# Kernel tuning notes

Hardware: AMD Instinct MI355X
Metric: run time of the kernel (lower is better)

The kernel has to match this reference:

```python
import jax, jax.numpy as jnp
import numpy as np

B, S, HID = 1, 2048, 2048
H, KVH, D = 32, 8, 64
NUM_MASKS = 3
ROPE_THETA = 10000.0


def rope_tables(seq_len, dim, theta=ROPE_THETA):
    inv_freq = 1.0 / (theta ** (np.arange(0, dim, 2, dtype=np.float32) / dim))
    t = np.arange(seq_len, dtype=np.float32)
    freqs = np.outer(t, inv_freq)                      # [S, D/2]
    emb = np.concatenate([freqs, freqs], axis=-1)      # [S, D]
    return jnp.asarray(np.cos(emb))[None], jnp.asarray(np.sin(emb))[None]  # [1,S,D]


def setup_inputs() -> dict:
    key = jax.random.key(0)
    ks = jax.random.split(key, 5)
    cos, sin = rope_tables(S, D)
    sc = 1.0 / np.sqrt(HID)
    return {
        "hidden_states": jax.random.normal(ks[0], (B, S, HID), jnp.float32),
        "cos": cos, "sin": sin,
        "Wq": jax.random.normal(ks[1], (HID, H * D), jnp.float32) * sc,
        "Wk": jax.random.normal(ks[2], (HID, KVH * D), jnp.float32) * sc,
        "Wv": jax.random.normal(ks[3], (HID, KVH * D), jnp.float32) * sc,
        "Wo": jax.random.normal(ks[4], (H * D, HID), jnp.float32) * sc,
        "num_masks": NUM_MASKS,
    }


def rotate_half(x):
    x1, x2 = jnp.split(x, 2, axis=-1)
    return jnp.concatenate([-x2, x1], axis=-1)


def block_causal_bias(seq_len, num_mask, dtype):
    block_size = num_mask + 1
    i = jnp.arange(seq_len)[:, None]
    j = jnp.arange(seq_len)[None, :]
    causal = j <= i
    column = causal & (j % (num_mask + 1) == 0)
    block = causal & ((i // block_size) == (j // block_size))
    allowed = column | block
    neg = jnp.asarray(jnp.finfo(dtype).min if dtype != jnp.float32 else -jnp.inf, dtype)
    return jnp.where(allowed, jnp.asarray(0.0, dtype), neg)  # [S,S]


def reference(hidden_states, cos, sin, Wq, Wk, Wv, Wo, num_masks):
    b, s, _ = hidden_states.shape
    scaling = D ** -0.5
    # projections -> [B, heads, S, D]
    q = (hidden_states @ Wq).reshape(b, s, H, D).transpose(0, 2, 1, 3)
    k = (hidden_states @ Wk).reshape(b, s, KVH, D).transpose(0, 2, 1, 3)
    v = (hidden_states @ Wv).reshape(b, s, KVH, D).transpose(0, 2, 1, 3)
    # RoPE (cos/sin: [1,S,D] -> [1,1,S,D])
    c, sn = cos[:, None], sin[:, None]
    q = q * c + rotate_half(q) * sn
    k = k * c + rotate_half(k) * sn
    # GQA: repeat kv heads
    g = H // KVH
    k = jnp.repeat(k, g, axis=1)
    v = jnp.repeat(v, g, axis=1)
    bias = block_causal_bias(s, num_masks, hidden_states.dtype)  # [S,S]
    scores = jnp.einsum("bhqd,bhkd->bhqk", q, k) * scaling + bias[None, None]
    probs = jax.nn.softmax(scores, axis=-1)
    out = jnp.einsum("bhqk,bhkd->bhqd", probs, v)  # [B,H,S,D]
    out = out.transpose(0, 2, 1, 3).reshape(b, s, H * D)
    return out @ Wo
```

## Files before the change

### kernel.cpp

```cpp
#include <hip/hip_runtime.h>
#include <hip/hip_bf16.h>
#include <stdint.h>

#define S_LEN  2048
#define HIDDEN 2048
#define NH     32
#define NKVH   8
#define HD     64
#define NHD    (NH*HD)
#define KVD    (NKVH*HD)

typedef __attribute__((ext_vector_type(8))) short  short8;
typedef __attribute__((ext_vector_type(4))) short  short4v;
typedef __attribute__((ext_vector_type(4))) float  f32x4;
typedef __attribute__((ext_vector_type(4))) float  float4v;
typedef __attribute__((ext_vector_type(8))) __bf16 bf16x8;

__device__ __forceinline__ short f2bf(float x){
  uint32_t u = __builtin_bit_cast(uint32_t, x);
  u += 0x7fffu + ((u >> 16) & 1u);
  return (short)(u >> 16);
}

__device__ __forceinline__ f32x4 mfma_bf16(short8 a, short8 b, f32x4 c){
  return __builtin_amdgcn_mfma_f32_16x16x32_bf16(
      __builtin_bit_cast(bf16x8, a), __builtin_bit_cast(bf16x8, b), c, 0, 0, 0);
}

__device__ __forceinline__ void gload16(const short* g, short* l){
  __builtin_amdgcn_global_load_lds(
      (const __attribute__((address_space(1))) void*)g,
      (__attribute__((address_space(3))) void*)l, 16, 0, 0);
}

__global__ __launch_bounds__(256) void k_prep(const float* __restrict__ hs,
                                              short* __restrict__ hsb,
                                              const float* __restrict__ Wq, short* __restrict__ WqT,
                                              const float* __restrict__ Wk, short* __restrict__ WkT,
                                              const float* __restrict__ Wv, short* __restrict__ WvT,
                                              const float* __restrict__ Wo, short* __restrict__ WoT){
  int bid = blockIdx.x;
  if (bid < 4096){
    int i = bid*256 + threadIdx.x;
    float4v v = ((const float4v* __restrict__)hs)[i];
    short4v o;
#pragma unroll
    for (int j=0;j<4;j++) o[j] = f2bf(v[j]);
    ((short4v* __restrict__)hsb)[i] = o;
    return;
  }
  bid -= 4096;
  const float* W; short* WT; int R, C, GX;
  if (bid < 4096)      { W = Wq; WT = WqT; R = HIDDEN; C = NHD; GX = 64; }
  else if (bid < 5120) { bid -= 4096; W = Wk; WT = WkT; R = HIDDEN; C = KVD; GX = 16; }
  else if (bid < 6144) { bid -= 5120; W = Wv; WT = WvT; R = HIDDEN; C = KVD; GX = 16; }
  else                 { bid -= 6144; W = Wo; WT = WoT; R = NHD; C = HIDDEN; GX = 64; }
  const int bx = bid % GX, by = bid / GX;
  __shared__ float tile[32][33];
  const int x = threadIdx.x & 31, y0 = threadIdx.x >> 5;
  const int c0 = bx*32, r0 = by*32;
#pragma unroll
  for (int yy=y0; yy<32; yy+=8) tile[yy][x] = W[(size_t)(r0+yy)*C + c0 + x];
  __syncthreads();
#pragma unroll
  for (int yy=y0; yy<32; yy+=8) WT[(size_t)(c0+yy)*R + r0 + x] = f2bf(tile[x][yy]);
}

struct GemmIdx {
  int wid, r, g, wr, wc, kg, gtid;
};
__device__ __forceinline__ GemmIdx gemm_idx(){
  GemmIdx ix;
  int tid = threadIdx.x, lane = tid&63;
  ix.kg = tid>>8; ix.gtid = tid&255;
  ix.wid = (tid>>6)&3; ix.r = lane&15; ix.g = lane>>4;
  ix.wr = ix.wid>>1; ix.wc = ix.wid&1;
  return ix;
}

__device__ __forceinline__ void stage128(const short* gA, const short* gB,
                                         short* As, short* Bs, int kt, int w){
  const int K = HIDDEN;
  gload16(gA + kt*32,                As + w*512);
  gload16(gA + (size_t)64*K + kt*32, As + 2048 + w*512);
  gload16(gB + kt*32,                Bs + w*512);
  gload16(gB + (size_t)64*K + kt*32, Bs + 2048 + w*512);
}

__device__ __forceinline__ void compute128(const short* As, const short* Bs,
                                           f32x4 acc[4][4], const GemmIdx& ix){
  short8 af[4], bf[4];
#pragma unroll
  for (int m=0;m<4;m++) af[m] = *(const short8*)&As[(ix.wr*64 + m*16 + ix.r)*32 + ix.g*8];
#pragma unroll
  for (int n=0;n<4;n++) bf[n] = *(const short8*)&Bs[(ix.wc*64 + n*16 + ix.r)*32 + ix.g*8];
#pragma unroll
  for (int m=0;m<4;m++)
#pragma unroll
    for (int n=0;n<4;n++) acc[m][n] = mfma_bf16(af[m], bf[n], acc[m][n]);
}

template<int NKT>
__device__ __forceinline__ void gemm_core512(const short* __restrict__ A,
                                             const short* __restrict__ BT,
                                             int bm, int bn, int kbase, short* LDS,
                                             f32x4 acc[4][4], const GemmIdx& ix){
  const int K = HIDDEN;
  const short* gA = A  + (size_t)(bm*128 + (ix.gtid>>2))*K + kbase + ix.kg*(NKT*32) + (ix.gtid&3)*8;
  const short* gB = BT + (size_t)(bn*128 + (ix.gtid>>2))*K + kbase + ix.kg*(NKT*32) + (ix.gtid&3)*8;
  short* L   = LDS + ix.kg*16384;
  short* As0 = L;        short* Bs0 = L + 4096;
  short* As1 = L + 8192; short* Bs1 = L + 12288;
  const int w = ix.gtid>>6;

#pragma unroll
  for (int m=0;m<4;m++)
#pragma unroll
    for (int n=0;n<4;n++) acc[m][n] = (f32x4){0.f,0.f,0.f,0.f};

  stage128(gA, gB, As0, Bs0, 0, w);
  __syncthreads();
  for (int u=0; u<NKT/2; ++u){
    const int t = 2*u;
    if (t+1 < NKT) stage128(gA, gB, As1, Bs1, t+1, w);
    compute128(As0, Bs0, acc, ix);
    __syncthreads();
    if (t+2 < NKT) stage128(gA, gB, As0, Bs0, t+2, w);
    compute128(As1, Bs1, acc, ix);
    __syncthreads();
  }

  float* red = (float*)LDS;
  if (ix.kg){
#pragma unroll
    for (int m=0;m<4;m++)
#pragma unroll
      for (int n=0;n<4;n++)
#pragma unroll
        for (int j=0;j<4;j++)
          red[ix.wid*4096 + (m*16 + ix.g*4 + j)*64 + n*16 + ix.r] = acc[m][n][j];
  }
  __syncthreads();
  if (!ix.kg){
#pragma unroll
    for (int m=0;m<4;m++)
#pragma unroll
      for (int n=0;n<4;n++)
#pragma unroll
        for (int j=0;j<4;j++)
          acc[m][n][j] += red[ix.wid*4096 + (m*16 + ix.g*4 + j)*64 + n*16 + ix.r];
  }
}

__global__ __launch_bounds__(512, 4) void k_gemm_qkv(const short* __restrict__ hsb,
                                                     const short* __restrict__ WqT,
                                                     const short* __restrict__ WkT,
                                                     const short* __restrict__ WvT,
                                                     const float* __restrict__ cosT,
                                                     const float* __restrict__ sinT,
                                                     const int* __restrict__ nm,
                                                     short* __restrict__ Qb,
                                                     short* __restrict__ Kb,
                                                     short* __restrict__ VT,
                                                     short* __restrict__ VTs){
  __shared__ short LDS[32768];
  const int bn = blockIdx.x, bm = blockIdx.y;
  GemmIdx ix = gemm_idx();
  f32x4 acc[4][4];

  if (bn < 16){
    gemm_core512<32>(hsb, WqT + (size_t)bn*128*HIDDEN, bm, 0, 0, LDS, acc, ix);
    if (ix.kg) return;
    const int h2 = bn*2 + ix.wc;
#pragma unroll
    for (int m=0;m<4;m++)
#pragma unroll
      for (int j=0;j<4;j++){
        const int s = bm*128 + ix.wr*64 + m*16 + ix.g*4 + j;
        const float* cr = cosT + s*64;
        const float* sr = sinT + s*64;
#pragma unroll
        for (int n=0;n<2;n++){
          const int d = n*16 + ix.r;
          float x1 = acc[m][n][j], x2 = acc[m][n+2][j];
          Qb[(size_t)s*NHD + h2*64 + d]      = f2bf((x1*cr[d]    - x2*sr[d])   *0.125f);
          Qb[(size_t)s*NHD + h2*64 + d + 32] = f2bf((x2*cr[d+32] + x1*sr[d+32])*0.125f);
        }
      }
  } else if (bn < 20){
    gemm_core512<32>(hsb, WkT + (size_t)(bn-16)*128*HIDDEN, bm, 0, 0, LDS, acc, ix);
    if (ix.kg) return;
    const int h2 = (bn-16)*2 + ix.wc;
#pragma unroll
    for (int m=0;m<4;m++)
#pragma unroll
      for (int j=0;j<4;j++){
        const int s = bm*128 + ix.wr*64 + m*16 + ix.g*4 + j;
        const float* cr = cosT + s*64;
        const float* sr = sinT + s*64;
#pragma unroll
        for (int n=0;n<2;n++){
          const int d = n*16 + ix.r;
          float x1 = acc[m][n][j], x2 = acc[m][n+2][j];
          Kb[(size_t)s*KVD + h2*64 + d]      = f2bf(x1*cr[d]    - x2*sr[d]);
          Kb[(size_t)s*KVD + h2*64 + d + 32] = f2bf(x2*cr[d+32] + x1*sr[d+32]);
        }
      }
  } else {
    gemm_core512<32>(hsb, WvT + (size_t)(bn-20)*128*HIDDEN, bm, 0, 0, LDS, acc, ix);
    if (ix.kg) return;
    const int bs  = nm[0] + 1;
    const int c0  = (bn-20)*128 + ix.wc*64;
    const int s0b = bm*128 + ix.wr*64 + ix.g*4;
    const int md  = s0b % bs;
    const int b0  = (s0b - md)/bs;
    const int d16 = 16/bs;
    bool mj[4]; int tj[4];
#pragma unroll
    for (int j=0;j<4;j++){
      int v = md + j;
      mj[j] = (v==0)||(v==bs)||(v==2*bs)||(v==3*bs);
      tj[j] = (v>=3*bs)?3:((v>=2*bs)?2:((v>=bs)?1:0));
    }
#pragma unroll
    for (int m=0;m<4;m++){
      const int sm = s0b + m*16;
#pragma unroll
      for (int n=0;n<4;n++){
        const int d = c0 + n*16 + ix.r;
        short4v o;
#pragma unroll
        for (int j=0;j<4;j++) o[j] = f2bf(acc[m][n][j]);
        *(short4v*)&VT[(size_t)d*S_LEN + sm] = o;
#pragma unroll
        for (int j=0;j<4;j++)
          if (mj[j]) VTs[(size_t)d*S_LEN + b0 + m*d16 + tj[j]] = o[j];
      }
    }
  }
}

__global__ __launch_bounds__(512, 4) void k_gemm(const short* __restrict__ A,
                                                 const short* __restrict__ BT,
                                                 float* __restrict__ C, int Nc){
  __shared__ short LDS[32768];
  const int bn = blockIdx.x, bm = blockIdx.y;
  GemmIdx ix = gemm_idx();
  f32x4 acc[4][4];
  gemm_core512<32>(A, BT, bm, bn, 0, LDS, acc, ix);
  if (ix.kg) return;
#pragma unroll
  for (int m=0;m<4;m++)
#pragma unroll
    for (int n=0;n<4;n++)
#pragma unroll
      for (int j=0;j<4;j++)
        C[(size_t)(bm*128 + ix.wr*64 + m*16 + ix.g*4 + j)*Nc
          + bn*128 + ix.wc*64 + n*16 + ix.r] = acc[m][n][j];
}


__device__ __forceinline__ void sm_pv1(f32x4 sc[4],
                                       float mrow[4], float lrow[4],
                                       f32x4 acc[4], short* Pw,
                                       const short* Vtile,
                                       int r, int g){
#pragma unroll
  for (int j=0;j<4;j++){
    float v = fmaxf(fmaxf(sc[0][j], sc[1][j]), fmaxf(sc[2][j], sc[3][j]));
    v = fmaxf(v, __shfl_xor(v, 1));
    v = fmaxf(v, __shfl_xor(v, 2));
    v = fmaxf(v, __shfl_xor(v, 4));
    v = fmaxf(v, __shfl_xor(v, 8));
    float mn = fmaxf(mrow[j], v);
    float fac = __expf(mrow[j] - mn);
    mrow[j] = mn;
#pragma unroll
    for (int f=0;f<4;f++) acc[f][j] *= fac;
    float rs = 0.f;
#pragma unroll
    for (int n=0;n<4;n++){
      float p = __expf(sc[n][j] - mn);
      rs += p;
      sc[n][j] = p;
    }
    rs += __shfl_xor(rs, 1);
    rs += __shfl_xor(rs, 2);
    rs += __shfl_xor(rs, 4);
    rs += __shfl_xor(rs, 8);
    lrow[j] = lrow[j]*fac + rs;
  }
#pragma unroll
  for (int n=0;n<4;n++)
#pragma unroll
    for (int j=0;j<4;j++)
      Pw[(g*4+j)*72 + n*16 + r] = f2bf(sc[n][j]);

  short8 pf0 = *(short8*)&Pw[r*72 + g*8];
  short8 pf1 = *(short8*)&Pw[r*72 + 32 + g*8];
#pragma unroll
  for (int f=0;f<4;f++){
    short8 vf0 = *(const short8*)(Vtile + (size_t)(f*16 + r)*S_LEN + g*8);
    short8 vf1 = *(const short8*)(Vtile + (size_t)(f*16 + r)*S_LEN + 32 + g*8);
    acc[f] = mfma_bf16(pf0, vf0, acc[f]);
    acc[f] = mfma_bf16(pf1, vf1, acc[f]);
  }
}

__global__ __launch_bounds__(64, 4) void k_attn3(const short* __restrict__ Qb,
                                                 const short* __restrict__ Kb,
                                                 const short* __restrict__ VT,
                                                 const short* __restrict__ VTs,
                                                 const int* __restrict__ nm,
                                                 short* __restrict__ Ob){
  const int i  = gridDim.x - 1 - blockIdx.x;
  const int qs = i >> 5;
  const int h  = i & 31;
  const int hk = h >> 2;
  const int bs = nm[0] + 1;

  const int lane = threadIdx.x;
  const int r = lane&15, g = lane>>4;

  __shared__ short Pw[16*72];

  const int qlo = qs*16;

  short8 qf0 = *(const short8*)(Qb + (size_t)(qlo + r)*NHD + h*HD + g*8);
  short8 qf1 = *(const short8*)(Qb + (size_t)(qlo + r)*NHD + h*HD + 32 + g*8);

  f32x4 acc[4];
  float mrow[4], lrow[4];
#pragma unroll
  for (int f=0;f<4;f++) acc[f] = (f32x4){0.f,0.f,0.f,0.f};
#pragma unroll
  for (int j=0;j<4;j++){ mrow[j] = -1e30f; lrow[j] = 0.f; }

  const short* Kg  = Kb  + hk*HD;
  const short* Vsg = VTs + (size_t)hk*HD*S_LEN;
  const short* Vdg = VT  + (size_t)hk*HD*S_LEN;

  const int cmax = qlo / bs;
  const int nct = (cmax + 63) >> 6;
  for (int ct=0; ct<nct; ++ct){
    const int cbase = ct*64;
    f32x4 sc[4];
#pragma unroll
    for (int n=0;n<4;n++){
      const int key = bs*(cbase + n*16 + r);
      short8 kf0 = *(const short8*)(Kg + (size_t)key*KVD + g*8);
      short8 kf1 = *(const short8*)(Kg + (size_t)key*KVD + 32 + g*8);
      f32x4 z = (f32x4){0.f,0.f,0.f,0.f};
      z = mfma_bf16(qf0, kf0, z);
      sc[n] = mfma_bf16(qf1, kf1, z);
    }
    if (cmax - cbase < 64){
#pragma unroll
      for (int n=0;n<4;n++){
        if (cbase + n*16 + r >= cmax){
#pragma unroll
          for (int j=0;j<4;j++) sc[n][j] = -1e30f;
        }
      }
    }
    sm_pv1(sc, mrow, lrow, acc, Pw, Vsg + cbase, r, g);
  }

  {
    const int key = qlo + r;
    short8 kf0 = *(const short8*)(Kg + (size_t)key*KVD + g*8);
    short8 kf1 = *(const short8*)(Kg + (size_t)key*KVD + 32 + g*8);
    f32x4 z = (f32x4){0.f,0.f,0.f,0.f};
    z = mfma_bf16(qf0, kf0, z);
    f32x4 sc0 = mfma_bf16(qf1, kf1, z);

    const int rb = r / bs, rm = r % bs;
#pragma unroll
    for (int j=0;j<4;j++){
      const int qrel = g*4 + j;
      bool ok = (r <= qrel) && ((rm == 0) || (rb == qrel/bs));
      sc0[j] = ok ? sc0[j] : -1e30f;
    }

#pragma unroll
    for (int j=0;j<4;j++){
      float v = sc0[j];
      v = fmaxf(v, __shfl_xor(v, 1));
      v = fmaxf(v, __shfl_xor(v, 2));
      v = fmaxf(v, __shfl_xor(v, 4));
      v = fmaxf(v, __shfl_xor(v, 8));
      float mn = fmaxf(mrow[j], v);
      float fac = __expf(mrow[j] - mn);
      mrow[j] = mn;
#pragma unroll
      for (int f=0;f<4;f++) acc[f][j] *= fac;
      float p = __expf(sc0[j] - mn);
      sc0[j] = p;
      float rs = p;
      rs += __shfl_xor(rs, 1);
      rs += __shfl_xor(rs, 2);
      rs += __shfl_xor(rs, 4);
      rs += __shfl_xor(rs, 8);
      lrow[j] = lrow[j]*fac + rs;
    }
#pragma unroll
    for (int j=0;j<4;j++){
      Pw[(g*4+j)*72 + r]      = f2bf(sc0[j]);
      Pw[(g*4+j)*72 + 16 + r] = 0;
    }
    short8 pf0 = *(short8*)&Pw[r*72 + g*8];
#pragma unroll
    for (int f=0;f<4;f++){
      short8 vf0 = *(const short8*)(Vdg + (size_t)(f*16 + r)*S_LEN + qlo + g*8);
      acc[f] = mfma_bf16(pf0, vf0, acc[f]);
    }
  }

#pragma unroll
  for (int j=0;j<4;j++){
    float inv = 1.f / lrow[j];
    const int q = qlo + g*4 + j;
#pragma unroll
    for (int f=0;f<4;f++)
      Ob[(size_t)q*NHD + h*HD + f*16 + r] = f2bf(acc[f][j]*inv);
  }
}

extern "C" void kernel_launch(void* const* d_in, const int* in_sizes, int n_in,
                              void* d_out, int out_size, void* d_ws, size_t ws_size,
                              hipStream_t stream){
  const float* hs   = (const float*)d_in[0];
  const float* cosT = (const float*)d_in[1];
  const float* sinT = (const float*)d_in[2];
  const float* Wq   = (const float*)d_in[3];
  const float* Wk   = (const float*)d_in[4];
  const float* Wv   = (const float*)d_in[5];
  const float* Wo   = (const float*)d_in[6];
  const int*   nm   = (const int*)d_in[7];

  char* ws = (char*)d_ws;
  short* hsb  = (short*)(ws);
  short* WqT  = (short*)(ws + (8ull<<20));
  short* WkT  = (short*)(ws + (16ull<<20));
  short* WvT  = (short*)(ws + (18ull<<20));
  short* WoT  = (short*)(ws + (20ull<<20));
  short* Qb   = (short*)(ws + (28ull<<20));
  short* Kb   = (short*)(ws + (36ull<<20));
  short* VT   = (short*)(ws + (38ull<<20));
  short* VTs  = (short*)(ws + (40ull<<20));
  short* attnb= (short*)(ws + (42ull<<20));
  float* out  = (float*)d_out;

  k_prep<<<dim3(14336), 256, 0, stream>>>(hs, hsb, Wq, WqT, Wk, WkT, Wv, WvT, Wo, WoT);

  k_gemm_qkv<<<dim3(24, 16), 512, 0, stream>>>(hsb, WqT, WkT, WvT, cosT, sinT, nm,
                                               Qb, Kb, VT, VTs);

  k_attn3<<<dim3((S_LEN/16)*NH), 64, 0, stream>>>(Qb, Kb, VT, VTs, nm, attnb);

  k_gemm<<<dim3(NHD/128, S_LEN/128), 512, 0, stream>>>(attnb, WoT, out, HIDDEN);
}
```

Before: 136.2 us.

## Split-K four ways in output GEMM and stage V transpose through LDS

The output projection GEMM now uses 1024-thread blocks with four K-groups of 16 tiles each, reducing partial sums through LDS in sequence. This raises per-CU wave count for the 256-block grid, at the cost of extra reduction barriers and double the LDS. The V epilogue in the QKV kernel now writes the tile transposed into LDS, then emits coalesced 16-byte VT stores and a strided-gather VTs. The VTs path computes the block size with a log2, so it assumes the block size is a power of two.

```diff
diff --git a/kernel.cpp b/kernel.cpp
--- a/kernel.cpp
+++ b/kernel.cpp
@@ -100,14 +100,14 @@
     for (int n=0;n<4;n++) acc[m][n] = mfma_bf16(af[m], bf[n], acc[m][n]);
 }
 
-template<int NKT>
+template<int NG, int NKT>
 __device__ __forceinline__ void gemm_core512(const short* __restrict__ A,
                                              const short* __restrict__ BT,
-                                             int bm, int bn, int kbase, short* LDS,
+                                             int bm, int bn, short* LDS,
                                              f32x4 acc[4][4], const GemmIdx& ix){
   const int K = HIDDEN;
-  const short* gA = A  + (size_t)(bm*128 + (ix.gtid>>2))*K + kbase + ix.kg*(NKT*32) + (ix.gtid&3)*8;
-  const short* gB = BT + (size_t)(bn*128 + (ix.gtid>>2))*K + kbase + ix.kg*(NKT*32) + (ix.gtid&3)*8;
+  const short* gA = A  + (size_t)(bm*128 + (ix.gtid>>2))*K + ix.kg*(NKT*32) + (ix.gtid&3)*8;
+  const short* gB = BT + (size_t)(bn*128 + (ix.gtid>>2))*K + ix.kg*(NKT*32) + (ix.gtid&3)*8;
   short* L   = LDS + ix.kg*16384;
   short* As0 = L;        short* Bs0 = L + 4096;
   short* As1 = L + 8192; short* Bs1 = L + 12288;
@@ -131,24 +131,28 @@
   }
 
   float* red = (float*)LDS;
-  if (ix.kg){
-#pragma unroll
-    for (int m=0;m<4;m++)
-#pragma unroll
-      for (int n=0;n<4;n++)
-#pragma unroll
-        for (int j=0;j<4;j++)
-          red[ix.wid*4096 + (m*16 + ix.g*4 + j)*64 + n*16 + ix.r] = acc[m][n][j];
-  }
-  __syncthreads();
-  if (!ix.kg){
-#pragma unroll
-    for (int m=0;m<4;m++)
-#pragma unroll
-      for (int n=0;n<4;n++)
-#pragma unroll
-        for (int j=0;j<4;j++)
-          acc[m][n][j] += red[ix.wid*4096 + (m*16 + ix.g*4 + j)*64 + n*16 + ix.r];
+#pragma unroll
+  for (int src=1; src<NG; ++src){
+    __syncthreads();
+    if (ix.kg == src){
+#pragma unroll
+      for (int m=0;m<4;m++)
+#pragma unroll
+        for (int n=0;n<4;n++)
+#pragma unroll
+          for (int j=0;j<4;j++)
+            red[ix.wid*4096 + (m*16 + ix.g*4 + j)*64 + n*16 + ix.r] = acc[m][n][j];
+    }
+    __syncthreads();
+    if (ix.kg == 0){
+#pragma unroll
+      for (int m=0;m<4;m++)
+#pragma unroll
+        for (int n=0;n<4;n++)
+#pragma unroll
+          for (int j=0;j<4;j++)
+            acc[m][n][j] += red[ix.wid*4096 + (m*16 + ix.g*4 + j)*64 + n*16 + ix.r];
+    }
   }
 }
 
@@ -169,7 +173,7 @@
   f32x4 acc[4][4];
 
   if (bn < 16){
-    gemm_core512<32>(hsb, WqT + (size_t)bn*128*HIDDEN, bm, 0, 0, LDS, acc, ix);
+    gemm_core512<2,32>(hsb, WqT + (size_t)bn*128*HIDDEN, bm, 0, LDS, acc, ix);
     if (ix.kg) return;
     const int h2 = bn*2 + ix.wc;
 #pragma unroll
@@ -188,7 +192,7 @@
         }
       }
   } else if (bn < 20){
-    gemm_core512<32>(hsb, WkT + (size_t)(bn-16)*128*HIDDEN, bm, 0, 0, LDS, acc, ix);
+    gemm_core512<2,32>(hsb, WkT + (size_t)(bn-16)*128*HIDDEN, bm, 0, LDS, acc, ix);
     if (ix.kg) return;
     const int h2 = (bn-16)*2 + ix.wc;
 #pragma unroll
@@ -207,47 +211,50 @@
         }
       }
   } else {
-    gemm_core512<32>(hsb, WvT + (size_t)(bn-20)*128*HIDDEN, bm, 0, 0, LDS, acc, ix);
-    if (ix.kg) return;
+    gemm_core512<2,32>(hsb, WvT + (size_t)(bn-20)*128*HIDDEN, bm, 0, LDS, acc, ix);
     const int bs  = nm[0] + 1;
-    const int c0  = (bn-20)*128 + ix.wc*64;
-    const int s0b = bm*128 + ix.wr*64 + ix.g*4;
-    const int md  = s0b % bs;
-    const int b0  = (s0b - md)/bs;
-    const int d16 = 16/bs;
-    bool mj[4]; int tj[4];
-#pragma unroll
-    for (int j=0;j<4;j++){
-      int v = md + j;
-      mj[j] = (v==0)||(v==bs)||(v==2*bs)||(v==3*bs);
-      tj[j] = (v>=3*bs)?3:((v>=2*bs)?2:((v>=bs)?1:0));
-    }
-#pragma unroll
-    for (int m=0;m<4;m++){
-      const int sm = s0b + m*16;
+    const int lbs = 31 - __clz(bs);
+    const int d0  = (bn-20)*128;
+    const int s0  = bm*128;
+    short* Vt = LDS;
+    __syncthreads();
+    if (!ix.kg){
 #pragma unroll
       for (int n=0;n<4;n++){
-        const int d = c0 + n*16 + ix.r;
-        short4v o;
-#pragma unroll
-        for (int j=0;j<4;j++) o[j] = f2bf(acc[m][n][j]);
-        *(short4v*)&VT[(size_t)d*S_LEN + sm] = o;
-#pragma unroll
-        for (int j=0;j<4;j++)
-          if (mj[j]) VTs[(size_t)d*S_LEN + b0 + m*d16 + tj[j]] = o[j];
+        const int dr = ix.wc*64 + n*16 + ix.r;
+#pragma unroll
+        for (int m=0;m<4;m++){
+          const int sc_ = ix.wr*64 + m*16 + ix.g*4;
+          short4v o;
+#pragma unroll
+          for (int j=0;j<4;j++) o[j] = f2bf(acc[m][n][j]);
+          *(short4v*)&Vt[dr*136 + sc_] = o;
+        }
       }
     }
-  }
-}
-
-__global__ __launch_bounds__(512, 4) void k_gemm(const short* __restrict__ A,
-                                                 const short* __restrict__ BT,
-                                                 float* __restrict__ C, int Nc){
-  __shared__ short LDS[32768];
+    __syncthreads();
+    const int tid = threadIdx.x;
+#pragma unroll
+    for (int it=0; it<4; ++it){
+      const int row = tid>>2, c8 = (tid&3)*32 + it*8;
+      *(short8*)&VT[(size_t)(d0+row)*S_LEN + s0 + c8] = *(short8*)&Vt[row*136 + c8];
+    }
+    const int cnt = 128 >> lbs;
+    for (int e = tid; e < 128*cnt; e += 512){
+      const int row = e >> (7 - lbs), c = e & (cnt - 1);
+      VTs[(size_t)(d0+row)*S_LEN + (s0>>lbs) + c] = Vt[row*136 + (c<<lbs)];
+    }
+  }
+}
+
+__global__ __launch_bounds__(1024, 4) void k_gemm(const short* __restrict__ A,
+                                                  const short* __restrict__ BT,
+                                                  float* __restrict__ C, int Nc){
+  __shared__ short LDS[65536];
   const int bn = blockIdx.x, bm = blockIdx.y;
   GemmIdx ix = gemm_idx();
   f32x4 acc[4][4];
-  gemm_core512<32>(A, BT, bm, bn, 0, LDS, acc, ix);
+  gemm_core512<4,16>(A, BT, bm, bn, LDS, acc, ix);
   if (ix.kg) return;
 #pragma unroll
   for (int m=0;m<4;m++)
@@ -458,5 +465,5 @@
 
   k_attn3<<<dim3((S_LEN/16)*NH), 64, 0, stream>>>(Qb, Kb, VT, VTs, nm, attnb);
 
-  k_gemm<<<dim3(NHD/128, S_LEN/128), 512, 0, stream>>>(attnb, WoT, out, HIDDEN);
-}
+  k_gemm<<<dim3(NHD/128, S_LEN/128), 1024, 0, stream>>>(attnb, WoT, out, HIDDEN);
+}
```

Measured after the change: 130.8 us. 1.04x faster.
